# Performance work log

Hardware: AMD Instinct MI355X
Metric: run time of the kernel (lower is better)

Reference implementation:

```python
import jax, jax.numpy as jnp
import numpy as np
import math

SEQ_LEN = 1024
NUM_FILTERS = 24
INPUT_DIM = 256
OUTPUT_DIM = 256
BATCH = 4


def _spectral_filters(seq_len, K):
    # Hankel matrix Z[i,j] = 2 / ((i+j)^3 - (i+j)), i,j in 1..L (use_hankel_L=False)
    entries = np.arange(1, seq_len + 1, dtype=np.float64)
    ipj = entries[:, None] + entries[None, :]
    Z = 2.0 / (ipj ** 3 - ipj)
    sigma, phi = np.linalg.eigh(Z)
    phi_k = phi[:, -K:] * (sigma[-K:] ** 0.25)
    return jnp.asarray(phi_k, dtype=jnp.float32)  # [L, K]


def setup_inputs() -> dict:
    key = jax.random.key(0)
    k1, k2, k3 = jax.random.split(key, 3)
    scale = (NUM_FILTERS * INPUT_DIM) ** (-0.5)
    x = jax.random.normal(k1, (BATCH, SEQ_LEN, INPUT_DIM), dtype=jnp.float32)
    phi = _spectral_filters(SEQ_LEN, NUM_FILTERS)
    M_phi_plus = jax.random.normal(k2, (NUM_FILTERS, INPUT_DIM, OUTPUT_DIM), dtype=jnp.float32) * scale
    M_phi_minus = jax.random.normal(k3, (NUM_FILTERS, INPUT_DIM, OUTPUT_DIM), dtype=jnp.float32) * scale
    return {"x": x, "phi": phi, "M_phi_plus": M_phi_plus, "M_phi_minus": M_phi_minus}


def reference(x, phi, M_phi_plus, M_phi_minus):
    B, L, I = x.shape
    n = 1 << math.ceil(math.log2(2 * L - 1))  # FFT length (2048 for L=1024)
    # alternating sign: +1 at even positions, -1 at odd (sgn[:,1::2] *= -1)
    sgn = jnp.where(jnp.arange(L) % 2 == 1, -1.0, 1.0).astype(jnp.float32)
    # FFT of filters: [F, K]
    V = jnp.fft.rfft(phi.astype(jnp.float32), n=n, axis=0)
    # FFT of input and sign-modulated input: [B, F, I]
    X = jnp.fft.rfft(x, n=n, axis=1)
    Xs = jnp.fft.rfft(x * sgn[None, :, None], n=n, axis=1)
    # pointwise multiply in frequency, broadcast over K: [B, F, K, I]
    U_plus = jnp.fft.irfft(V[None, :, :, None] * X[:, :, None, :], n=n, axis=1)[:, :L]
    U_minus = jnp.fft.irfft(V[None, :, :, None] * Xs[:, :, None, :], n=n, axis=1)[:, :L]
    U_minus = U_minus * sgn[None, :, None, None]
    # spectral projection: [B, L, O]
    out = jnp.einsum('blki,kio->blo', U_plus, M_phi_plus)
    out = out + jnp.einsum('blki,kio->blo', U_minus, M_phi_minus)
    return out
```

## Files before the change

kernel.cpp:

```cpp
#include <hip/hip_runtime.h>


#define ZB_ 12582912

typedef __attribute__((ext_vector_type(8))) short bf16x8;
typedef __attribute__((ext_vector_type(4))) float f32x4;

__device__ inline unsigned short f2bf(float f) {
    unsigned u = __float_as_uint(f);
    u += 0x7FFFu + ((u >> 16) & 1u);
    return (unsigned short)(u >> 16);
}

__device__ inline float bf2f(unsigned short s) {
    unsigned u = ((unsigned)s) << 16;
    return __uint_as_float(u);
}

__device__ inline void gl16(const unsigned short* g, unsigned short* l) {
    __builtin_amdgcn_global_load_lds((const __attribute__((address_space(1))) void*)g,
                                     (__attribute__((address_space(3))) void*)l, 16, 0, 0);
}

__global__ __launch_bounds__(256) void k_prep_all(const float* __restrict__ x,
                                                  const float* __restrict__ phi,
                                                  const float* __restrict__ Mp,
                                                  const float* __restrict__ Mm,
                                                  unsigned short* __restrict__ xb,
                                                  unsigned short* __restrict__ ToepA,
                                                  unsigned short* __restrict__ MbT) {
    __shared__ float tile[32][33];
    int bid = blockIdx.x, tid = threadIdx.x;
    if (bid < 1024) {
        int i = (bid * 256 + tid) * 4;
        float4 v = *(const float4*)(x + i);
        ushort4 o;
        o.x = f2bf(v.x); o.y = f2bf(v.y); o.z = f2bf(v.z); o.w = f2bf(v.w);
        int row = i >> 8, col = i & 255;
        int dst = (row << 8) | (col & 224) | ((col & 31) ^ (((row >> 1) & 3) << 3));
        *(ushort4*)(xb + dst) = o;
    } else if (bid < 1792) {
        int r = bid - 1024;
        int kk = r >> 4;
        int dm = (r & 15) - 1;
        int k = (kk < 24) ? kk : kk - 24;
        int i = tid >> 1, j0 = (tid & 1) * 32;
        unsigned short* dst = ToepA + ((size_t)kk * 16 + (dm + 1)) * 8192 + i * 64;
        int sw = (i & 7) << 3;
#pragma unroll
        for (int q = 0; q < 8; ++q) {
            int j = j0 + q * 4;
            unsigned short e[4];
#pragma unroll
            for (int ee = 0; ee < 4; ++ee) {
                int t = dm * 64 + i - (j + ee);
                float v = 0.f;
                if (t >= 0 && t < 1024) {
                    v = phi[t * 24 + k];
                    if (kk >= 24 && (t & 1)) v = -v;
                }
                e[ee] = f2bf(v);
            }
            ushort4 ov; ov.x = e[0]; ov.y = e[1]; ov.z = e[2]; ov.w = e[3];
            *(ushort4*)(dst + (j ^ sw)) = ov;
        }
    } else {
        int flat = bid - 1792;
        int kk = flat >> 6, rr = flat & 63;
        int i0 = (rr >> 3) * 32, o0 = (rr & 7) * 32;
        int tx = tid & 31, ty = tid >> 5;
        const float* src = ((kk < 24) ? Mp : Mm) + (size_t)((kk < 24) ? kk : kk - 24) * 65536;
        for (int j = 0; j < 4; ++j)
            tile[ty + j * 8][tx] = src[(i0 + ty + j * 8) * 256 + o0 + tx];
        __syncthreads();
        for (int j = 0; j < 4; ++j) {
            int orow = o0 + ty + j * 8, i = i0 + tx;
            int ic = (i & 224) | ((i & 31) ^ (((orow >> 1) & 3) << 3));
            MbT[(size_t)kk * 65536 + orow * 256 + ic] = f2bf(tile[tx][ty + j * 8]);
        }
    }
}

__global__ __launch_bounds__(256, 4) void k_stage1(const unsigned short* __restrict__ xb0,
                                                   const unsigned short* __restrict__ MbT,
                                                   unsigned short* __restrict__ Z) {
    __shared__ unsigned short Ab[2][4096];
    __shared__ unsigned short Bb[3][4096];
    int tid = threadIdx.x, lane = tid & 63, w = tid >> 6;
    int wm = w >> 1, wn = w & 1;

    int nwg = 768 * gridDim.z;
    int orig = blockIdx.x + blockIdx.y * 8 + blockIdx.z * 768;
    int wg = (orig & 7) * (nwg >> 3) + (orig >> 3);
    int m0 = (wg & 7) * 128;
    int rem = wg >> 3;
    int yy = rem % 96;
    int b  = rem / 96;
    int kk = yy >> 1;
    int o0 = (yy & 1) * 128;

    const unsigned short* xb_b = xb0 + (size_t)b * 262144;
    unsigned short* Zb = Z + (size_t)b * ZB_;
    const unsigned short* Bsrc = MbT + (size_t)kk * 65536;
    int l16 = lane & 15, kofs = (lane >> 4) * 8;
    int sw32 = ((l16 >> 1) & 3) << 3;
    int r4l = lane >> 2, c4 = (lane & 3) * 8;

    int arow[2], brow[2], lofs[2];
#pragma unroll
    for (int q = 0; q < 2; ++q) {
        int rr = q * 64 + w * 16 + r4l;
        arow[q] = (m0 + rr) * 256 + c4;
        brow[q] = (o0 + rr) * 256 + c4;
        lofs[q] = q * 2048 + w * 512;
    }

    f32x4 acc[4][4];
    for (int i = 0; i < 4; ++i)
        for (int j = 0; j < 4; ++j) {
            acc[i][j][0] = 0.f; acc[i][j][1] = 0.f; acc[i][j][2] = 0.f; acc[i][j][3] = 0.f;
        }

    auto stageA = [&](int bi, int ko) {
#pragma unroll
        for (int q = 0; q < 2; ++q) gl16(xb_b + arow[q] + ko * 32, &Ab[bi][0] + lofs[q]);
    };
    auto stageB = [&](int bi, int ko) {
#pragma unroll
        for (int q = 0; q < 2; ++q) gl16(Bsrc + brow[q] + ko * 32, &Bb[bi][0] + lofs[q]);
    };

    stageA(0, 0); stageB(0, 0); stageB(1, 1);

    for (int ko = 0; ko < 8; ++ko) {
        if (ko < 7) { asm volatile("s_waitcnt vmcnt(2)" ::: "memory"); }
        else        { asm volatile("s_waitcnt vmcnt(0)" ::: "memory"); }
        __builtin_amdgcn_sched_barrier(0);
        __builtin_amdgcn_s_barrier();
        __builtin_amdgcn_sched_barrier(0);
        if (ko < 7) stageA((ko + 1) & 1, ko + 1);
        if (ko < 6) stageB((ko + 2) % 3, ko + 2);

        const unsigned short* Abase = &Ab[ko & 1][0];
        const unsigned short* Bbase = &Bb[ko % 3][0];
        int koX = kofs ^ sw32;
        bf16x8 af[4], bfv[4];
#pragma unroll
        for (int mi = 0; mi < 4; ++mi)
            af[mi] = *(const bf16x8*)(Abase + (wm * 64 + mi * 16 + l16) * 32 + koX);
#pragma unroll
        for (int ni = 0; ni < 4; ++ni)
            bfv[ni] = *(const bf16x8*)(Bbase + (wn * 64 + ni * 16 + l16) * 32 + koX);
        __builtin_amdgcn_s_setprio(1);
#pragma unroll
        for (int mi = 0; mi < 4; ++mi)
#pragma unroll
            for (int ni = 0; ni < 4; ++ni)
                acc[mi][ni] = __builtin_amdgcn_mfma_f32_16x16x32_bf16(af[mi], bfv[ni], acc[mi][ni], 0, 0, 0);
        __builtin_amdgcn_s_setprio(0);
    }

    int r4 = (lane >> 4) * 4;
    for (int mi = 0; mi < 4; ++mi) {
        int sbase = m0 + wm * 64 + mi * 16 + r4;
        for (int ni = 0; ni < 4; ++ni) {
            int o = o0 + wn * 64 + ni * 16 + l16;
            ushort4 pk;
            pk.x = f2bf(acc[mi][ni][0]); pk.y = f2bf(acc[mi][ni][1]);
            pk.z = f2bf(acc[mi][ni][2]); pk.w = f2bf(acc[mi][ni][3]);
            *(ushort4*)(Zb + (size_t)kk * 262144 + (size_t)o * 1024 + (sbase ^ ((o & 7) << 3))) = pk;
        }
    }
}

__global__ __launch_bounds__(256, 2) void k_stage2(const unsigned short* __restrict__ Z,
                                                   const unsigned short* __restrict__ ToepA,
                                                   unsigned short* __restrict__ partial, int kkpg) {
    __shared__ unsigned short Abuf[2][8192];
    __shared__ unsigned short Zbuf[3][8192];
    int tid = threadIdx.x, lane = tid & 63, w = tid >> 6;
    int wm = w >> 1, wn = w & 1;

    int gy = gridDim.y, nwg = 4 * gy * gridDim.z;
    int orig = blockIdx.x + blockIdx.y * 4 + blockIdx.z * 4 * gy;
    int wg = (orig & 7) * (nwg >> 3) + (orig >> 3);
    int pr = wg & 3;
    int yy = (wg >> 2) % gy;
    int zz = (wg >> 2) / gy;
    int o0 = (yy & 1) * 128;
    int b  = yy >> 1;
    int kgi = zz;
    int kk0 = kgi * kkpg;

    int l16 = lane & 15, kofs = (lane >> 4) * 8;
    int sw = (l16 & 7) << 3;
    int r8 = lane >> 3, cg = lane & 7;

    const unsigned short* Zb = Z + (size_t)b * ZB_;
    unsigned short* pb = partial + ((size_t)b * gridDim.z + kgi) * 262144;

    int arow[4], zrow[4], lofs[4];
#pragma unroll
    for (int q = 0; q < 4; ++q) {
        int rr = q * 32 + w * 8 + r8;
        arow[q] = rr * 64 + cg * 8;
        zrow[q] = (o0 + rr) * 1024 + cg * 8;
        lofs[q] = q * 2048 + w * 512;
    }

    for (int half = 0; half < 2; ++half) {
        int lb = half ? (7 - pr) : pr;
        int l0 = lb * 128;
        int nch = 2 * lb + 2;
        int total = kkpg * nch;

        f32x4 acc[4][4];
        for (int i = 0; i < 4; ++i)
            for (int j = 0; j < 4; ++j) {
                acc[i][j][0] = 0.f; acc[i][j][1] = 0.f; acc[i][j][2] = 0.f; acc[i][j][3] = 0.f;
            }

        __syncthreads();

        auto stageA = [&](int bi, int kka, int didx) {
            const unsigned short* gA = ToepA + ((size_t)kka * 16 + didx) * 8192;
#pragma unroll
            for (int q = 0; q < 4; ++q) gl16(gA + arow[q], &Abuf[bi][0] + lofs[q]);
        };
        auto stageZ = [&](int bi, int kka, int s0) {
            const unsigned short* gZ = Zb + (size_t)kka * 262144 + s0;
#pragma unroll
            for (int q = 0; q < 4; ++q) gl16(gZ + zrow[q], &Zbuf[bi][0] + lofs[q]);
        };
        auto compute = [&](int ba, int bz) {
            const unsigned short* Abase = &Abuf[ba][0];
            const unsigned short* Zbase = &Zbuf[bz][0];
            __builtin_amdgcn_s_setprio(1);
#pragma unroll
            for (int ks = 0; ks < 2; ++ks) {
                int koX = (ks * 32 + kofs) ^ sw;
                bf16x8 af[4], bfv[4];
#pragma unroll
                for (int mi = 0; mi < 4; ++mi)
                    af[mi] = *(const bf16x8*)(Abase + (wm * 64 + mi * 16 + l16) * 64 + koX);
#pragma unroll
                for (int ni = 0; ni < 4; ++ni)
                    bfv[ni] = *(const bf16x8*)(Zbase + (wn * 64 + ni * 16 + l16) * 64 + koX);
#pragma unroll
                for (int mi = 0; mi < 4; ++mi)
#pragma unroll
                    for (int ni = 0; ni < 4; ++ni)
                        acc[mi][ni] = __builtin_amdgcn_mfma_f32_16x16x32_bf16(af[mi], bfv[ni], acc[mi][ni], 0, 0, 0);
            }
            __builtin_amdgcn_s_setprio(0);
        };

        stageA(0, kk0, 2 * lb + 1);
        stageZ(0, kk0, 0);
        stageZ(1, kk0, 64);

        int scA = 1, kkA = 0;
        int scZ = 2, kkZ = 0;
        if (scZ == nch) { scZ = 0; kkZ = 1; }
        int jz = 2;

        for (int j = 0; j < total - 1; ++j) {
            asm volatile("s_waitcnt vmcnt(4)" ::: "memory");
            __builtin_amdgcn_sched_barrier(0);
            __builtin_amdgcn_s_barrier();
            __builtin_amdgcn_sched_barrier(0);
            stageA((j + 1) & 1, kk0 + kkA, 2 * lb - scA + 1);
            ++scA; if (scA == nch) { scA = 0; ++kkA; }
            if (jz < total) {
                stageZ(jz % 3, kk0 + kkZ, scZ * 64);
                ++scZ; if (scZ == nch) { scZ = 0; ++kkZ; }
                ++jz;
            }
            compute(j & 1, j % 3);
        }
        asm volatile("s_waitcnt vmcnt(0)" ::: "memory");
        __builtin_amdgcn_sched_barrier(0);
        __builtin_amdgcn_s_barrier();
        __builtin_amdgcn_sched_barrier(0);
        compute((total - 1) & 1, (total - 1) % 3);

        int r4 = (lane >> 4) * 4;
        for (int mi = 0; mi < 4; ++mi) {
            int l = l0 + wm * 64 + mi * 16 + r4;
            for (int ni = 0; ni < 4; ++ni) {
                int o = o0 + wn * 64 + ni * 16 + l16;
                unsigned short* dst = pb + (size_t)l * 256 + o;
                dst[0]   = f2bf(acc[mi][ni][0]);
                dst[256] = f2bf(acc[mi][ni][1]);
                dst[512] = f2bf(acc[mi][ni][2]);
                dst[768] = f2bf(acc[mi][ni][3]);
            }
        }
    }
}

__global__ void k_reduce(const unsigned short* __restrict__ partial, float* __restrict__ outg, int kg) {
    const unsigned short* pb = partial + (size_t)blockIdx.y * kg * 262144;
    int i = (blockIdx.x * 256 + threadIdx.x) * 8;
    float s[8];
#pragma unroll
    for (int j = 0; j < 8; ++j) s[j] = 0.f;
    for (int kgi = 0; kgi < kg; ++kgi) {
        uint4 v = *(const uint4*)(pb + (size_t)kgi * 262144 + i);
        unsigned vv[4] = {v.x, v.y, v.z, v.w};
#pragma unroll
        for (int q = 0; q < 4; ++q) {
            s[q * 2]     += bf2f((unsigned short)(vv[q] & 0xFFFF));
            s[q * 2 + 1] += bf2f((unsigned short)(vv[q] >> 16));
        }
    }
    float4 o0, o1;
    o0.x = s[0]; o0.y = s[1]; o0.z = s[2]; o0.w = s[3];
    o1.x = s[4]; o1.y = s[5]; o1.z = s[6]; o1.w = s[7];
    float* dst = outg + (size_t)blockIdx.y * 262144 + i;
    *(float4*)(dst) = o0;
    *(float4*)(dst + 4) = o1;
}

extern "C" void kernel_launch(void* const* d_in, const int* in_sizes, int n_in,
                              void* d_out, int out_size, void* d_ws, size_t ws_size,
                              hipStream_t stream) {
    const float* x   = (const float*)d_in[0];
    const float* phi = (const float*)d_in[1];
    const float* Mp  = (const float*)d_in[2];
    const float* Mm  = (const float*)d_in[3];
    float* out = (float*)d_out;

    char* ws = (char*)d_ws;
    unsigned short* xb    = (unsigned short*)(ws);
    unsigned short* MbT   = (unsigned short*)(ws + 2097152);
    unsigned short* ToepA = (unsigned short*)(ws + 8388608);
    unsigned short* Zbuf  = (unsigned short*)(ws + 20971520);
    const size_t fixed = 20971520;

    int g = 4, kg = 16;
    auto need = [&](int gg, int kk) {
        return fixed + (size_t)gg * 25165824 + (size_t)gg * (size_t)kk * 524288;
    };
    if (need(4, 16) > ws_size) {
        kg = 12;
        if (need(4, 12) > ws_size) {
            g = 2; kg = 16;
            if (need(2, 16) > ws_size) {
                kg = 12;
                if (need(2, 12) > ws_size) {
                    g = 1; kg = 16;
                    if (need(1, 16) > ws_size) {
                        kg = 12;
                        if (need(1, 12) > ws_size) kg = 6;
                    }
                }
            }
        }
    }
    unsigned short* partial = (unsigned short*)(ws + fixed + (size_t)g * 25165824);

    k_prep_all<<<dim3(4864), dim3(256), 0, stream>>>(x, phi, Mp, Mm, xb, ToepA, MbT);

    for (int b0 = 0; b0 < 4; b0 += g) {
        k_stage1<<<dim3(8, 96, g), dim3(256), 0, stream>>>(xb + (size_t)b0 * 262144, MbT, Zbuf);
        k_stage2<<<dim3(4, 2 * g, kg), dim3(256), 0, stream>>>(Zbuf, ToepA, partial, 48 / kg);
        k_reduce<<<dim3(128, g), dim3(256), 0, stream>>>(partial, out + (size_t)b0 * 262144, kg);
    }
}
```

Measured before the change: 130.7 us.

## Widen stage2 tile to full 256 outputs with 512-thread blocks sharing A tile

The Toeplitz-projection GEMM kernel now uses 512-thread workgroups covering all 256 output columns, so each staged A (Toeplitz) tile is shared across twice as many outputs. Grid size halves in y. The pipeline changes from a double-buffered A plus triple-buffered Z to a single A buffer plus double-buffered Z, with an extra barrier between compute and the next load. This aims to cut redundant A loads and LDS traffic, but loses some load/compute overlap and halves the number of workgroups, which may reduce occupancy.

Measured after the change: 141.3 us. +8.1%, slower.

```diff
diff --git a/kernel.cpp b/kernel.cpp
--- a/kernel.cpp
+++ b/kernel.cpp
@@ -173,40 +173,32 @@
     }
 }
 
-__global__ __launch_bounds__(256, 2) void k_stage2(const unsigned short* __restrict__ Z,
+__global__ __launch_bounds__(512, 4) void k_stage2(const unsigned short* __restrict__ Z,
                                                    const unsigned short* __restrict__ ToepA,
                                                    unsigned short* __restrict__ partial, int kkpg) {
-    __shared__ unsigned short Abuf[2][8192];
-    __shared__ unsigned short Zbuf[3][8192];
+    __shared__ unsigned short Abuf[8192];
+    __shared__ unsigned short Zbuf[2][16384];
     int tid = threadIdx.x, lane = tid & 63, w = tid >> 6;
-    int wm = w >> 1, wn = w & 1;
-
-    int gy = gridDim.y, nwg = 4 * gy * gridDim.z;
-    int orig = blockIdx.x + blockIdx.y * 4 + blockIdx.z * 4 * gy;
+    int wm = w >> 2, wn = w & 3;
+
+    int nwg = 4 * gridDim.y * gridDim.z;
+    int orig = blockIdx.x + blockIdx.y * 4 + blockIdx.z * 4 * gridDim.y;
     int wg = (orig & 7) * (nwg >> 3) + (orig >> 3);
     int pr = wg & 3;
-    int yy = (wg >> 2) % gy;
-    int zz = (wg >> 2) / gy;
-    int o0 = (yy & 1) * 128;
-    int b  = yy >> 1;
-    int kgi = zz;
+    int rem = wg >> 2;
+    int b   = rem % gridDim.y;
+    int kgi = rem / gridDim.y;
     int kk0 = kgi * kkpg;
 
     int l16 = lane & 15, kofs = (lane >> 4) * 8;
     int sw = (l16 & 7) << 3;
-    int r8 = lane >> 3, cg = lane & 7;
 
     const unsigned short* Zb = Z + (size_t)b * ZB_;
     unsigned short* pb = partial + ((size_t)b * gridDim.z + kgi) * 262144;
 
-    int arow[4], zrow[4], lofs[4];
-#pragma unroll
-    for (int q = 0; q < 4; ++q) {
-        int rr = q * 32 + w * 8 + r8;
-        arow[q] = rr * 64 + cg * 8;
-        zrow[q] = (o0 + rr) * 1024 + cg * 8;
-        lofs[q] = q * 2048 + w * 512;
-    }
+    int r0 = tid >> 3, cg = (tid & 7) * 8;
+    int zg0 = r0 * 1024 + cg;
+    int zl0 = r0 * 64 + cg;
 
     for (int half = 0; half < 2; ++half) {
         int lb = half ? (7 - pr) : pr;
@@ -222,18 +214,19 @@
 
         __syncthreads();
 
-        auto stageA = [&](int bi, int kka, int didx) {
-            const unsigned short* gA = ToepA + ((size_t)kka * 16 + didx) * 8192;
-#pragma unroll
-            for (int q = 0; q < 4; ++q) gl16(gA + arow[q], &Abuf[bi][0] + lofs[q]);
+        auto stageA = [&](int kkx, int sc) {
+            const unsigned short* gA = ToepA + ((size_t)(kk0 + kkx) * 16 + (2 * lb - sc + 1)) * 8192;
+            gl16(gA + zl0, Abuf + zl0);
+            gl16(gA + zl0 + 4096, Abuf + zl0 + 4096);
         };
-        auto stageZ = [&](int bi, int kka, int s0) {
-            const unsigned short* gZ = Zb + (size_t)kka * 262144 + s0;
-#pragma unroll
-            for (int q = 0; q < 4; ++q) gl16(gZ + zrow[q], &Zbuf[bi][0] + lofs[q]);
+        auto stageZ = [&](int bi, int kkx, int sc) {
+            const unsigned short* gZ = Zb + (size_t)(kk0 + kkx) * 262144 + sc * 64;
+            unsigned short* lz = &Zbuf[bi][0];
+#pragma unroll
+            for (int q = 0; q < 4; ++q)
+                gl16(gZ + zg0 + q * 65536, lz + zl0 + q * 4096);
         };
-        auto compute = [&](int ba, int bz) {
-            const unsigned short* Abase = &Abuf[ba][0];
+        auto compute = [&](int bz) {
             const unsigned short* Zbase = &Zbuf[bz][0];
             __builtin_amdgcn_s_setprio(1);
 #pragma unroll
@@ -242,7 +235,7 @@
                 bf16x8 af[4], bfv[4];
 #pragma unroll
                 for (int mi = 0; mi < 4; ++mi)
-                    af[mi] = *(const bf16x8*)(Abase + (wm * 64 + mi * 16 + l16) * 64 + koX);
+                    af[mi] = *(const bf16x8*)(Abuf + (wm * 64 + mi * 16 + l16) * 64 + koX);
 #pragma unroll
                 for (int ni = 0; ni < 4; ++ni)
                     bfv[ni] = *(const bf16x8*)(Zbase + (wn * 64 + ni * 16 + l16) * 64 + koX);
@@ -255,40 +248,39 @@
             __builtin_amdgcn_s_setprio(0);
         };
 
-        stageA(0, kk0, 2 * lb + 1);
-        stageZ(0, kk0, 0);
-        stageZ(1, kk0, 64);
+        stageA(0, 0);
+        stageZ(0, 0, 0);
+        stageZ(1, 0, 1);
 
         int scA = 1, kkA = 0;
         int scZ = 2, kkZ = 0;
         if (scZ == nch) { scZ = 0; kkZ = 1; }
-        int jz = 2;
-
-        for (int j = 0; j < total - 1; ++j) {
-            asm volatile("s_waitcnt vmcnt(4)" ::: "memory");
+
+        for (int j = 0; j < total; ++j) {
+            if (j < total - 1) { asm volatile("s_waitcnt vmcnt(4)" ::: "memory"); }
+            else               { asm volatile("s_waitcnt vmcnt(0)" ::: "memory"); }
             __builtin_amdgcn_sched_barrier(0);
             __builtin_amdgcn_s_barrier();
             __builtin_amdgcn_sched_barrier(0);
-            stageA((j + 1) & 1, kk0 + kkA, 2 * lb - scA + 1);
-            ++scA; if (scA == nch) { scA = 0; ++kkA; }
-            if (jz < total) {
-                stageZ(jz % 3, kk0 + kkZ, scZ * 64);
+            compute(j & 1);
+            __builtin_amdgcn_sched_barrier(0);
+            __builtin_amdgcn_s_barrier();
+            __builtin_amdgcn_sched_barrier(0);
+            if (j + 1 < total) {
+                stageA(kkA, scA);
+                ++scA; if (scA == nch) { scA = 0; ++kkA; }
+            }
+            if (j + 2 < total) {
+                stageZ(j & 1, kkZ, scZ);
                 ++scZ; if (scZ == nch) { scZ = 0; ++kkZ; }
-                ++jz;
-            }
-            compute(j & 1, j % 3);
-        }
-        asm volatile("s_waitcnt vmcnt(0)" ::: "memory");
-        __builtin_amdgcn_sched_barrier(0);
-        __builtin_amdgcn_s_barrier();
-        __builtin_amdgcn_sched_barrier(0);
-        compute((total - 1) & 1, (total - 1) % 3);
+            }
+        }
 
         int r4 = (lane >> 4) * 4;
         for (int mi = 0; mi < 4; ++mi) {
             int l = l0 + wm * 64 + mi * 16 + r4;
             for (int ni = 0; ni < 4; ++ni) {
-                int o = o0 + wn * 64 + ni * 16 + l16;
+                int o = wn * 64 + ni * 16 + l16;
                 unsigned short* dst = pb + (size_t)l * 256 + o;
                 dst[0]   = f2bf(acc[mi][ni][0]);
                 dst[256] = f2bf(acc[mi][ni][1]);
@@ -364,7 +356,7 @@
 
     for (int b0 = 0; b0 < 4; b0 += g) {
         k_stage1<<<dim3(8, 96, g), dim3(256), 0, stream>>>(xb + (size_t)b0 * 262144, MbT, Zbuf);
-        k_stage2<<<dim3(4, 2 * g, kg), dim3(256), 0, stream>>>(Zbuf, ToepA, partial, 48 / kg);
+        k_stage2<<<dim3(4, g, kg), dim3(512), 0, stream>>>(Zbuf, ToepA, partial, 48 / kg);
         k_reduce<<<dim3(128, g), dim3(256), 0, stream>>>(partial, out + (size_t)b0 * 262144, kg);
     }
 }
```

## Replace materialized Toeplitz tiles with compact filter table loaded directly into registers

Applied to the files above, without the earlier changes.

Stops materializing 64x64 Toeplitz blocks of the filters (12 MB) and instead stores a small reversed per-filter table with even/odd split copies. Stage 2 loads the A fragments straight from global memory into registers via unaligned 16-byte loads, which drops the A LDS double buffer. That frees shared memory for 3 blocks per CU and allows the k-split to rise to 24. The cost is uncoalesced, partly redundant global loads of A on every iteration and more partial-sum traffic for the reduce step.

Result: slower. 134.0 us (+2.5%).

```diff
diff --git a/kernel.cpp b/kernel.cpp
--- a/kernel.cpp
+++ b/kernel.cpp
@@ -5,6 +5,7 @@
 
 typedef __attribute__((ext_vector_type(8))) short bf16x8;
 typedef __attribute__((ext_vector_type(4))) float f32x4;
+typedef unsigned int uint4a __attribute__((ext_vector_type(4), aligned(4)));
 
 __device__ inline unsigned short f2bf(float f) {
     unsigned u = __float_as_uint(f);
@@ -20,6 +21,12 @@
 __device__ inline void gl16(const unsigned short* g, unsigned short* l) {
     __builtin_amdgcn_global_load_lds((const __attribute__((address_space(1))) void*)g,
                                      (__attribute__((address_space(3))) void*)l, 16, 0, 0);
+}
+
+__device__ inline bf16x8 ld16u(const unsigned short* p) {
+    union { uint4a u; bf16x8 b; } cv;
+    cv.u = *(const uint4a*)p;
+    return cv.b;
 }
 
 __global__ __launch_bounds__(256) void k_prep_all(const float* __restrict__ x,
@@ -27,7 +34,7 @@
                                                   const float* __restrict__ Mp,
                                                   const float* __restrict__ Mm,
                                                   unsigned short* __restrict__ xb,
-                                                  unsigned short* __restrict__ ToepA,
+                                                  unsigned short* __restrict__ Ptab,
                                                   unsigned short* __restrict__ MbT) {
     __shared__ float tile[32][33];
     int bid = blockIdx.x, tid = threadIdx.x;
@@ -39,33 +46,26 @@
         int row = i >> 8, col = i & 255;
         int dst = (row << 8) | (col & 224) | ((col & 31) ^ (((row >> 1) & 3) << 3));
         *(ushort4*)(xb + dst) = o;
-    } else if (bid < 1792) {
-        int r = bid - 1024;
-        int kk = r >> 4;
-        int dm = (r & 15) - 1;
+    } else if (bid < 1072) {
+        int kk = bid - 1024;
         int k = (kk < 24) ? kk : kk - 24;
-        int i = tid >> 1, j0 = (tid & 1) * 32;
-        unsigned short* dst = ToepA + ((size_t)kk * 16 + (dm + 1)) * 8192 + i * 64;
-        int sw = (i & 7) << 3;
-#pragma unroll
-        for (int q = 0; q < 8; ++q) {
-            int j = j0 + q * 4;
-            unsigned short e[4];
-#pragma unroll
-            for (int ee = 0; ee < 4; ++ee) {
-                int t = dm * 64 + i - (j + ee);
-                float v = 0.f;
-                if (t >= 0 && t < 1024) {
-                    v = phi[t * 24 + k];
-                    if (kk >= 24 && (t & 1)) v = -v;
-                }
-                e[ee] = f2bf(v);
-            }
-            ushort4 ov; ov.x = e[0]; ov.y = e[1]; ov.z = e[2]; ov.w = e[3];
-            *(ushort4*)(dst + (j ^ sw)) = ov;
+        bool neg = kk >= 24;
+        unsigned short* dst = Ptab + (size_t)kk * 2560;
+#pragma unroll
+        for (int it = 0; it < 10; ++it) {
+            int idx = it * 256 + tid;
+            int c = idx / 1280, i = idx - c * 1280;
+            int jj = i + c;
+            float v = 0.f;
+            if (jj <= 1023) {
+                int t = 1023 - jj;
+                v = phi[t * 24 + k];
+                if (neg && (t & 1)) v = -v;
+            }
+            dst[idx] = f2bf(v);
         }
     } else {
-        int flat = bid - 1792;
+        int flat = bid - 1072;
         int kk = flat >> 6, rr = flat & 63;
         int i0 = (rr >> 3) * 32, o0 = (rr & 7) * 32;
         int tx = tid & 31, ty = tid >> 5;
@@ -173,10 +173,9 @@
     }
 }
 
-__global__ __launch_bounds__(256, 2) void k_stage2(const unsigned short* __restrict__ Z,
-                                                   const unsigned short* __restrict__ ToepA,
+__global__ __launch_bounds__(256, 3) void k_stage2(const unsigned short* __restrict__ Z,
+                                                   const unsigned short* __restrict__ Ptab,
                                                    unsigned short* __restrict__ partial, int kkpg) {
-    __shared__ unsigned short Abuf[2][8192];
     __shared__ unsigned short Zbuf[3][8192];
     int tid = threadIdx.x, lane = tid & 63, w = tid >> 6;
     int wm = w >> 1, wn = w & 1;
@@ -195,15 +194,15 @@
     int l16 = lane & 15, kofs = (lane >> 4) * 8;
     int sw = (l16 & 7) << 3;
     int r8 = lane >> 3, cg = lane & 7;
+    int K0 = 1023 - (wm * 64 + l16) + kofs;
 
     const unsigned short* Zb = Z + (size_t)b * ZB_;
     unsigned short* pb = partial + ((size_t)b * gridDim.z + kgi) * 262144;
 
-    int arow[4], zrow[4], lofs[4];
+    int zrow[4], lofs[4];
 #pragma unroll
     for (int q = 0; q < 4; ++q) {
         int rr = q * 32 + w * 8 + r8;
-        arow[q] = rr * 64 + cg * 8;
         zrow[q] = (o0 + rr) * 1024 + cg * 8;
         lofs[q] = q * 2048 + w * 512;
     }
@@ -222,27 +221,30 @@
 
         __syncthreads();
 
-        auto stageA = [&](int bi, int kka, int didx) {
-            const unsigned short* gA = ToepA + ((size_t)kka * 16 + didx) * 8192;
-#pragma unroll
-            for (int q = 0; q < 4; ++q) gl16(gA + arow[q], &Abuf[bi][0] + lofs[q]);
-        };
-        auto stageZ = [&](int bi, int kka, int s0) {
-            const unsigned short* gZ = Zb + (size_t)kka * 262144 + s0;
+        auto stageZ = [&](int bi, int kkx, int sc) {
+            const unsigned short* gZ = Zb + (size_t)(kk0 + kkx) * 262144 + sc * 64;
 #pragma unroll
             for (int q = 0; q < 4; ++q) gl16(gZ + zrow[q], &Zbuf[bi][0] + lofs[q]);
         };
-        auto compute = [&](int ba, int bz) {
-            const unsigned short* Abase = &Abuf[ba][0];
+        auto aloadA = [&](bf16x8 (&dst)[4][2], int kkx, int sc) {
+            int dm = 2 * lb - sc;
+            const unsigned short* Pb = Ptab + (size_t)(kk0 + kkx) * 2560;
+#pragma unroll
+            for (int mi = 0; mi < 4; ++mi)
+#pragma unroll
+                for (int ks = 0; ks < 2; ++ks) {
+                    int u = K0 - dm * 64 - mi * 16 + ks * 32;
+                    int idx = (u & ~1) + ((u & 1) ? 1280 : 0);
+                    dst[mi][ks] = ld16u(Pb + idx);
+                }
+        };
+        auto compute = [&](bf16x8 (&afr)[4][2], int bz) {
             const unsigned short* Zbase = &Zbuf[bz][0];
             __builtin_amdgcn_s_setprio(1);
 #pragma unroll
             for (int ks = 0; ks < 2; ++ks) {
                 int koX = (ks * 32 + kofs) ^ sw;
-                bf16x8 af[4], bfv[4];
-#pragma unroll
-                for (int mi = 0; mi < 4; ++mi)
-                    af[mi] = *(const bf16x8*)(Abase + (wm * 64 + mi * 16 + l16) * 64 + koX);
+                bf16x8 bfv[4];
 #pragma unroll
                 for (int ni = 0; ni < 4; ++ni)
                     bfv[ni] = *(const bf16x8*)(Zbase + (wn * 64 + ni * 16 + l16) * 64 + koX);
@@ -250,39 +252,38 @@
                 for (int mi = 0; mi < 4; ++mi)
 #pragma unroll
                     for (int ni = 0; ni < 4; ++ni)
-                        acc[mi][ni] = __builtin_amdgcn_mfma_f32_16x16x32_bf16(af[mi], bfv[ni], acc[mi][ni], 0, 0, 0);
+                        acc[mi][ni] = __builtin_amdgcn_mfma_f32_16x16x32_bf16(afr[mi][ks], bfv[ni], acc[mi][ni], 0, 0, 0);
             }
             __builtin_amdgcn_s_setprio(0);
         };
 
-        stageA(0, kk0, 2 * lb + 1);
-        stageZ(0, kk0, 0);
-        stageZ(1, kk0, 64);
-
-        int scA = 1, kkA = 0;
+        bf16x8 aR[4][2];
+
+        stageZ(0, 0, 0);
+        {
+            int sc1 = 1 % nch, kk1 = 1 / nch;
+            stageZ(1, kk1, sc1);
+        }
+        int scC = 0, kkC = 0;
         int scZ = 2, kkZ = 0;
-        if (scZ == nch) { scZ = 0; kkZ = 1; }
+        if (scZ >= nch) { scZ -= nch; ++kkZ; }
         int jz = 2;
 
-        for (int j = 0; j < total - 1; ++j) {
-            asm volatile("s_waitcnt vmcnt(4)" ::: "memory");
+        for (int j = 0; j < total; ++j) {
+            aloadA(aR, kkC, scC);
+            ++scC; if (scC == nch) { scC = 0; ++kkC; }
+            if (j + 1 < total) { asm volatile("s_waitcnt vmcnt(12)" ::: "memory"); }
+            else               { asm volatile("s_waitcnt vmcnt(8)"  ::: "memory"); }
             __builtin_amdgcn_sched_barrier(0);
             __builtin_amdgcn_s_barrier();
             __builtin_amdgcn_sched_barrier(0);
-            stageA((j + 1) & 1, kk0 + kkA, 2 * lb - scA + 1);
-            ++scA; if (scA == nch) { scA = 0; ++kkA; }
             if (jz < total) {
-                stageZ(jz % 3, kk0 + kkZ, scZ * 64);
+                stageZ(jz % 3, kkZ, scZ);
                 ++scZ; if (scZ == nch) { scZ = 0; ++kkZ; }
                 ++jz;
             }
-            compute(j & 1, j % 3);
-        }
-        asm volatile("s_waitcnt vmcnt(0)" ::: "memory");
-        __builtin_amdgcn_sched_barrier(0);
-        __builtin_amdgcn_s_barrier();
-        __builtin_amdgcn_sched_barrier(0);
-        compute((total - 1) & 1, (total - 1) % 3);
+            compute(aR, j % 3);
+        }
 
         int r4 = (lane >> 4) * 4;
         for (int mi = 0; mi < 4; ++mi) {
@@ -332,27 +333,30 @@
     float* out = (float*)d_out;
 
     char* ws = (char*)d_ws;
-    unsigned short* xb    = (unsigned short*)(ws);
-    unsigned short* MbT   = (unsigned short*)(ws + 2097152);
-    unsigned short* ToepA = (unsigned short*)(ws + 8388608);
-    unsigned short* Zbuf  = (unsigned short*)(ws + 20971520);
-    const size_t fixed = 20971520;
-
-    int g = 4, kg = 16;
+    unsigned short* xb   = (unsigned short*)(ws);
+    unsigned short* MbT  = (unsigned short*)(ws + 2097152);
+    unsigned short* Ptab = (unsigned short*)(ws + 8388608);
+    unsigned short* Zbuf = (unsigned short*)(ws + 8912896);
+    const size_t fixed = 8912896;
+
+    int g = 4, kg = 24;
     auto need = [&](int gg, int kk) {
         return fixed + (size_t)gg * 25165824 + (size_t)gg * (size_t)kk * 524288;
     };
-    if (need(4, 16) > ws_size) {
-        kg = 12;
-        if (need(4, 12) > ws_size) {
-            g = 2; kg = 16;
-            if (need(2, 16) > ws_size) {
-                kg = 12;
-                if (need(2, 12) > ws_size) {
-                    g = 1; kg = 16;
-                    if (need(1, 16) > ws_size) {
-                        kg = 12;
-                        if (need(1, 12) > ws_size) kg = 6;
+    if (need(4, 24) > ws_size) {
+        kg = 16;
+        if (need(4, 16) > ws_size) {
+            kg = 12;
+            if (need(4, 12) > ws_size) {
+                g = 2; kg = 16;
+                if (need(2, 16) > ws_size) {
+                    kg = 12;
+                    if (need(2, 12) > ws_size) {
+                        g = 1; kg = 16;
+                        if (need(1, 16) > ws_size) {
+                            kg = 12;
+                            if (need(1, 12) > ws_size) kg = 6;
+                        }
                     }
                 }
             }
@@ -360,11 +364,11 @@
     }
     unsigned short* partial = (unsigned short*)(ws + fixed + (size_t)g * 25165824);
 
-    k_prep_all<<<dim3(4864), dim3(256), 0, stream>>>(x, phi, Mp, Mm, xb, ToepA, MbT);
+    k_prep_all<<<dim3(4144), dim3(256), 0, stream>>>(x, phi, Mp, Mm, xb, Ptab, MbT);
 
     for (int b0 = 0; b0 < 4; b0 += g) {
         k_stage1<<<dim3(8, 96, g), dim3(256), 0, stream>>>(xb + (size_t)b0 * 262144, MbT, Zbuf);
-        k_stage2<<<dim3(4, 2 * g, kg), dim3(256), 0, stream>>>(Zbuf, ToepA, partial, 48 / kg);
+        k_stage2<<<dim3(4, 2 * g, kg), dim3(256), 0, stream>>>(Zbuf, Ptab, partial, 48 / kg);
         k_reduce<<<dim3(128, g), dim3(256), 0, stream>>>(partial, out + (size_t)b0 * 262144, kg);
     }
 }
```

## Widen stage2 tile to full 256 output columns per workgroup

Applied to the files above, without the earlier changes.

Each stage2 workgroup now covers all 256 output columns for a 128-row block instead of 128. Every wave computes 128x64 with 8x4 MFMA accumulators, and the Z staging buffer doubles to 16K elements per slot. The grid halves in the y dimension, so each Toeplitz A tile is loaded once per batch rather than twice, which cuts A traffic and LDS A reads per FLOP. In exchange it doubles accumulator registers, raises LDS use, and lowers occupancy to one workgroup per CU with half as many workgroups.

New measurement: 150.7 us. +15.3%, slower.

```diff
diff --git a/kernel.cpp b/kernel.cpp
--- a/kernel.cpp
+++ b/kernel.cpp
@@ -173,39 +173,40 @@
     }
 }
 
-__global__ __launch_bounds__(256, 2) void k_stage2(const unsigned short* __restrict__ Z,
+__global__ __launch_bounds__(256, 1) void k_stage2(const unsigned short* __restrict__ Z,
                                                    const unsigned short* __restrict__ ToepA,
                                                    unsigned short* __restrict__ partial, int kkpg) {
     __shared__ unsigned short Abuf[2][8192];
-    __shared__ unsigned short Zbuf[3][8192];
+    __shared__ unsigned short Zbuf[3][16384];
     int tid = threadIdx.x, lane = tid & 63, w = tid >> 6;
-    int wm = w >> 1, wn = w & 1;
 
     int gy = gridDim.y, nwg = 4 * gy * gridDim.z;
     int orig = blockIdx.x + blockIdx.y * 4 + blockIdx.z * 4 * gy;
     int wg = (orig & 7) * (nwg >> 3) + (orig >> 3);
     int pr = wg & 3;
-    int yy = (wg >> 2) % gy;
-    int zz = (wg >> 2) / gy;
-    int o0 = (yy & 1) * 128;
-    int b  = yy >> 1;
-    int kgi = zz;
+    int rem = wg >> 2;
+    int b   = rem % gy;
+    int kgi = rem / gy;
     int kk0 = kgi * kkpg;
 
     int l16 = lane & 15, kofs = (lane >> 4) * 8;
     int sw = (l16 & 7) << 3;
-    int r8 = lane >> 3, cg = lane & 7;
 
     const unsigned short* Zb = Z + (size_t)b * ZB_;
     unsigned short* pb = partial + ((size_t)b * gridDim.z + kgi) * 262144;
 
-    int arow[4], zrow[4], lofs[4];
+    int r0 = tid >> 3, cg = (tid & 7) * 8;
+    int arow[4], lofsA[4];
 #pragma unroll
     for (int q = 0; q < 4; ++q) {
-        int rr = q * 32 + w * 8 + r8;
-        arow[q] = rr * 64 + cg * 8;
-        zrow[q] = (o0 + rr) * 1024 + cg * 8;
-        lofs[q] = q * 2048 + w * 512;
+        arow[q]  = (q * 32 + r0) * 64 + cg;
+        lofsA[q] = q * 2048 + (r0 * 64 + cg) - (r0 * 64 + cg) + (r0 * 64 + cg);
+    }
+    int zrow[8], lofsZ[8];
+#pragma unroll
+    for (int q = 0; q < 8; ++q) {
+        zrow[q]  = (q * 32 + r0) * 1024 + cg;
+        lofsZ[q] = q * 2048 + r0 * 64 + cg;
     }
 
     for (int half = 0; half < 2; ++half) {
@@ -214,8 +215,8 @@
         int nch = 2 * lb + 2;
         int total = kkpg * nch;
 
-        f32x4 acc[4][4];
-        for (int i = 0; i < 4; ++i)
+        f32x4 acc[8][4];
+        for (int i = 0; i < 8; ++i)
             for (int j = 0; j < 4; ++j) {
                 acc[i][j][0] = 0.f; acc[i][j][1] = 0.f; acc[i][j][2] = 0.f; acc[i][j][3] = 0.f;
             }
@@ -225,12 +226,12 @@
         auto stageA = [&](int bi, int kka, int didx) {
             const unsigned short* gA = ToepA + ((size_t)kka * 16 + didx) * 8192;
 #pragma unroll
-            for (int q = 0; q < 4; ++q) gl16(gA + arow[q], &Abuf[bi][0] + lofs[q]);
+            for (int q = 0; q < 4; ++q) gl16(gA + arow[q], &Abuf[bi][0] + lofsA[q]);
         };
         auto stageZ = [&](int bi, int kka, int s0) {
             const unsigned short* gZ = Zb + (size_t)kka * 262144 + s0;
 #pragma unroll
-            for (int q = 0; q < 4; ++q) gl16(gZ + zrow[q], &Zbuf[bi][0] + lofs[q]);
+            for (int q = 0; q < 8; ++q) gl16(gZ + zrow[q], &Zbuf[bi][0] + lofsZ[q]);
         };
         auto compute = [&](int ba, int bz) {
             const unsigned short* Abase = &Abuf[ba][0];
@@ -239,15 +240,15 @@
 #pragma unroll
             for (int ks = 0; ks < 2; ++ks) {
                 int koX = (ks * 32 + kofs) ^ sw;
-                bf16x8 af[4], bfv[4];
-#pragma unroll
-                for (int mi = 0; mi < 4; ++mi)
-                    af[mi] = *(const bf16x8*)(Abase + (wm * 64 + mi * 16 + l16) * 64 + koX);
+                bf16x8 af[8], bfv[4];
+#pragma unroll
+                for (int mi = 0; mi < 8; ++mi)
+                    af[mi] = *(const bf16x8*)(Abase + (mi * 16 + l16) * 64 + koX);
 #pragma unroll
                 for (int ni = 0; ni < 4; ++ni)
-                    bfv[ni] = *(const bf16x8*)(Zbase + (wn * 64 + ni * 16 + l16) * 64 + koX);
-#pragma unroll
-                for (int mi = 0; mi < 4; ++mi)
+                    bfv[ni] = *(const bf16x8*)(Zbase + (w * 64 + ni * 16 + l16) * 64 + koX);
+#pragma unroll
+                for (int mi = 0; mi < 8; ++mi)
 #pragma unroll
                     for (int ni = 0; ni < 4; ++ni)
                         acc[mi][ni] = __builtin_amdgcn_mfma_f32_16x16x32_bf16(af[mi], bfv[ni], acc[mi][ni], 0, 0, 0);
@@ -265,7 +266,7 @@
         int jz = 2;
 
         for (int j = 0; j < total - 1; ++j) {
-            asm volatile("s_waitcnt vmcnt(4)" ::: "memory");
+            asm volatile("s_waitcnt vmcnt(8)" ::: "memory");
             __builtin_amdgcn_sched_barrier(0);
             __builtin_amdgcn_s_barrier();
             __builtin_amdgcn_sched_barrier(0);
@@ -285,10 +286,10 @@
         compute((total - 1) & 1, (total - 1) % 3);
 
         int r4 = (lane >> 4) * 4;
-        for (int mi = 0; mi < 4; ++mi) {
-            int l = l0 + wm * 64 + mi * 16 + r4;
+        for (int mi = 0; mi < 8; ++mi) {
+            int l = l0 + mi * 16 + r4;
             for (int ni = 0; ni < 4; ++ni) {
-                int o = o0 + wn * 64 + ni * 16 + l16;
+                int o = w * 64 + ni * 16 + l16;
                 unsigned short* dst = pb + (size_t)l * 256 + o;
                 dst[0]   = f2bf(acc[mi][ni][0]);
                 dst[256] = f2bf(acc[mi][ni][1]);
@@ -364,7 +365,7 @@
 
     for (int b0 = 0; b0 < 4; b0 += g) {
         k_stage1<<<dim3(8, 96, g), dim3(256), 0, stream>>>(xb + (size_t)b0 * 262144, MbT, Zbuf);
-        k_stage2<<<dim3(4, 2 * g, kg), dim3(256), 0, stream>>>(Zbuf, ToepA, partial, 48 / kg);
+        k_stage2<<<dim3(4, g, kg), dim3(256), 0, stream>>>(Zbuf, ToepA, partial, 48 / kg);
         k_reduce<<<dim3(128, g), dim3(256), 0, stream>>>(partial, out + (size_t)b0 * 262144, kg);
     }
 }
```
